# Kernel tuning notes

Hardware: AMD Instinct MI355X
Metric: run time of the kernel (lower is better)

The kernel has to match this reference:

```python
import jax, jax.numpy as jnp
import numpy as np

# Module hyper-parameters (init_kwargs)
CLIPVAR = 5.0   # variance is clipped to this before confidence = exp(-var)
MAXRANGE = 16   # max integration radius (pixels) in each of 4 directions
LAM = 0.05      # blend factor between depthin and CRF lateral estimate
N_CLASSES = 19


def _shift(x, axis, d, fill):
    """d=+1: out[..., n] = x[..., n-1] (pad with fill); d=-1: out[..., n] = x[..., n+1]."""
    pad = [(0, 0)] * x.ndim
    idx = [slice(None)] * x.ndim
    L = x.shape[axis]
    if d > 0:
        pad[axis] = (1, 0)
        idx[axis] = slice(0, L)
    else:
        pad[axis] = (0, 1)
        idx[axis] = slice(1, L + 1)
    return jnp.pad(x, pad, constant_values=fill)[tuple(idx)]


def _dir_accum(g, sem, msk, var, dep, axis, d, pre_shift, sign, clipvar, R):
    """Accumulate confidence-weighted depth estimates propagated from up to R
    same-semantic neighbors along one direction. All arrays are [bz,h,w].
    Depth estimate from neighbor at offset s: dep[neighbor] * exp(signed path
    sum of log-gradients g along the traversal)."""
    zeros = jnp.zeros_like(dep)
    valid0 = (msk == 1)  # only masked centers receive contributions

    def step(carry, _):
        g_sh, sem_sh, msk_sh, var_sh, dep_sh, pathlog, valid, dsum, csum = carry
        if pre_shift:  # newly added gradient term lives at the neighbor pixel
            g_sh = _shift(g_sh, axis, d, 0.0)
            pathlog = pathlog + sign * g_sh
        else:          # newly added gradient term lives one step before neighbor
            pathlog = pathlog + sign * g_sh
            g_sh = _shift(g_sh, axis, d, 0.0)
        sem_sh = _shift(sem_sh, axis, d, -1)
        msk_sh = _shift(msk_sh, axis, d, 0)
        var_sh = _shift(var_sh, axis, d, 0.0)
        dep_sh = _shift(dep_sh, axis, d, 0.0)
        # traversal stops (stays stopped) at semantic boundary / invalid pixel
        valid = valid & (sem_sh == sem) & (msk_sh == 1)
        conf = jnp.where(valid, jnp.exp(-jnp.minimum(var_sh, clipvar)), 0.0)
        dsum = dsum + conf * dep_sh * jnp.exp(pathlog)
        csum = csum + conf
        return (g_sh, sem_sh, msk_sh, var_sh, dep_sh, pathlog, valid, dsum, csum), None

    carry0 = (g, sem, msk, var, dep, zeros, valid0, zeros, zeros)
    carry, _ = jax.lax.scan(step, carry0, None, length=R)
    return carry[-2], carry[-1]


def crf_integrate(pred_log, semantics, mask, variance, depthin, clipvar, R):
    g0 = pred_log[:, 0]  # horizontal log-gradient: log d[n+1] - log d[n]
    g1 = pred_log[:, 1]  # vertical   log-gradient: log d[m+1] - log d[m]
    sem = semantics[:, 0]
    msk = mask[:, 0]
    var = variance[:, 0]
    dep = depthin[:, 0]
    # self term
    selfconf = jnp.where(msk == 1, jnp.exp(-jnp.minimum(var, clipvar)), 0.0)
    dsum = selfconf * dep
    csum = selfconf
    # (gradient map, axis, shift dir, pre_shift_g, sign): left, right, up, down
    dirs = [(g0, 2, 1, True, 1.0), (g0, 2, -1, False, -1.0),
            (g1, 1, 1, True, 1.0), (g1, 1, -1, False, -1.0)]
    for g, axis, d, pre, sgn in dirs:
        ds, cs = _dir_accum(g, sem, msk, var, dep, axis, d, pre, sgn, clipvar, R)
        dsum = dsum + ds
        csum = csum + cs
    out = jnp.where(csum > 0, dsum / jnp.maximum(csum, 1e-12), 0.0)
    return out[:, None]  # [bz,1,h,w]


def setup_inputs() -> dict:
    key = jax.random.key(0)
    k1, k2, k3, k4, k5 = jax.random.split(key, 5)
    bz, h, w = 4, 256, 832
    pred_log = 0.1 * jax.random.normal(k1, (bz, 2, h, w), dtype=jnp.float32)
    semantics = jax.random.randint(k2, (bz, 1, h, w), 0, N_CLASSES, dtype=jnp.int32)
    mask = jax.random.randint(k3, (bz, 1, h, w), 0, 2, dtype=jnp.int32)
    variance = 5.0 * jax.random.uniform(k4, (bz, 1, h, w), dtype=jnp.float32)
    depthin = 0.5 + 10.0 * jax.random.uniform(k5, (bz, 1, h, w), dtype=jnp.float32)
    return {"pred_log": pred_log, "semantics": semantics, "mask": mask,
            "variance": variance, "depthin": depthin, "times": 1}


def reference(pred_log, semantics, mask, variance, depthin, times):
    depthout = depthin
    for _ in range(times):
        lateral = crf_integrate(pred_log, semantics, mask, variance, depthout,
                                 CLIPVAR, MAXRANGE)
        sel = (lateral > 0).astype(depthin.dtype)
        depthout = (1.0 - sel) * depthin + sel * (depthin * LAM + lateral * (1.0 - LAM))
    return depthout
```

## Files before the change

### kernel.cpp

```cpp
#include <hip/hip_runtime.h>

#define W 832
#define H 256
#define BZ 4
#define RR 16
#define LAM_C 0.05f

#define CT 32
#define S  64
#define NT 512
#define NBLK (26 * 8 * 4)


__device__ __forceinline__ unsigned bf16r(float x) {
    const unsigned u = __float_as_uint(x);
    return (u + 0x7FFFu + ((u >> 16) & 1u)) >> 16;
}
__device__ __forceinline__ float decCD(unsigned p) {
    return __uint_as_float(p & 0xFFFF0000u);
}
__device__ __forceinline__ float decCF(unsigned p) {
    return __uint_as_float(0x3B800000u + ((p & 0xFFE0u) << 11));
}

__global__ __launch_bounds__(NT) void k_fused(
    const float* __restrict__ pred_log, const int* __restrict__ sem,
    const int* __restrict__ msk, const float* __restrict__ var,
    const float* __restrict__ dep, float* __restrict__ out)
{
    __shared__ float    sG0[S * S];
    __shared__ unsigned sP1[S * S];
    __shared__ float    sG1[S * CT];

    const int orig = blockIdx.x;
    const int wg   = (orig & 7) * 104 + (orig >> 3);
    const int bz   = wg / 208;
    const int rem  = wg - bz * 208;
    const int by   = rem / 26;
    const int bx   = rem - by * 26;

    const int tid = threadIdx.x;
    const int c0 = bx * CT;
    const int r0 = by * CT;
    const size_t im0 = (size_t)bz * H * W;
    const size_t g0b = ((size_t)(bz * 2)) * H * W;
    const size_t g1b = ((size_t)(bz * 2 + 1)) * H * W;

    #pragma unroll
    for (int k = 0; k < 2; ++k) {
        const int q = tid + NT * k;
        const int sr = q >> 4;
        const int sc4 = (q & 15) << 2;
        const int rimg = r0 - RR + sr;
        const int cimg = c0 - RR + sc4;
        float4 g4 = make_float4(0.f, 0.f, 0.f, 0.f);
        uint4 p4 = make_uint4(31u, 31u, 31u, 31u);
        if (rimg >= 0 && rimg < H && cimg >= 0 && cimg < W) {
            const size_t off = im0 + (size_t)rimg * W + cimg;
            g4 = *reinterpret_cast<const float4*>(&pred_log[g0b + (size_t)rimg * W + cimg]);
            const int4   mk4 = *reinterpret_cast<const int4*>(&msk[off]);
            const int4   se4 = *reinterpret_cast<const int4*>(&sem[off]);
            const float4 vr4 = *reinterpret_cast<const float4*>(&var[off]);
            const float4 dp4 = *reinterpret_cast<const float4*>(&dep[off]);
            #pragma unroll
            for (int e = 0; e < 4; ++e) {
                const int   mk1 = (&mk4.x)[e];
                const float vr1 = (&vr4.x)[e];
                if (mk1 == 1) {
                    const float cf = __expf(-fminf(vr1, 5.f));
                    const unsigned enc = (__float_as_uint(cf) - 0x3B800000u + 0x8000u) >> 16;
                    (&p4.x)[e] = (bf16r(cf * (&dp4.x)[e]) << 16) | (enc << 5)
                               | (unsigned)(&se4.x)[e];
                }
            }
        }
        const int i = sr * S + sc4;
        *reinterpret_cast<float4*>(&sG0[i]) = g4;
        *reinterpret_cast<uint4*>(&sP1[i])  = p4;
    }
    {
        const int ar = tid >> 3;
        const int ac4 = (tid & 7) << 2;
        const int rimg = r0 - RR + ar;
        float4 g1q = make_float4(0.f, 0.f, 0.f, 0.f);
        if (rimg >= 0 && rimg < H)
            g1q = *reinterpret_cast<const float4*>(
                &pred_log[g1b + (size_t)rimg * W + c0 + ac4]);
        *reinterpret_cast<float4*>(&sG1[ar * CT + ac4]) = g1q;
    }
    __syncthreads();

    float dsA[4], csA[4];
    #pragma unroll
    for (int k = 0; k < 4; ++k) {
        const int row = (tid >> 5) + 16 * k;
        const int col = tid & 31;
        const int ci = row * S + RR + col;
        const unsigned uc = sP1[ci];
        const unsigned semc = uc & 31u;
        float ds = 0.0f, cs = 0.0f;
        if (semc != 31u) {
            ds = decCD(uc);
            cs = decCF(uc);
            float psum = 0.0f;
            #pragma unroll 1
            for (int s = 1; s <= RR; ++s) {
                const unsigned u = sP1[ci - s];
                if ((u & 31u) != semc) break;
                psum += sG0[ci - s];
                ds = fmaf(decCD(u), __expf(psum), ds);
                cs += decCF(u);
            }
            psum = 0.0f;
            #pragma unroll 1
            for (int s = 1; s <= RR; ++s) {
                const unsigned u = sP1[ci + s];
                if ((u & 31u) != semc) break;
                psum -= sG0[ci + s - 1];
                ds = fmaf(decCD(u), __expf(psum), ds);
                cs += decCF(u);
            }
        }
        dsA[k] = ds; csA[k] = cs;
    }

    #pragma unroll
    for (int j = 0; j < 2; ++j) {
        const int prow = (tid >> 5) + 16 * j;
        const int pcol = tid & 31;
        const int rs = prow + RR;
        const int ci = rs * S + RR + pcol;
        const int gi = rs * CT + pcol;
        const unsigned uc = sP1[ci];
        const unsigned semc = uc & 31u;
        const size_t off = im0 + (size_t)(r0 + prow) * W + (c0 + pcol);
        const float dpin = dep[off];
        float ds = dsA[j + 1], cs = csA[j + 1];
        if (semc != 31u) {
            float psum = 0.0f;
            #pragma unroll 1
            for (int s = 1; s <= RR; ++s) {
                const unsigned u = sP1[ci - s * S];
                if ((u & 31u) != semc) break;
                psum += sG1[gi - s * CT];
                ds = fmaf(decCD(u), __expf(psum), ds);
                cs += decCF(u);
            }
            psum = 0.0f;
            #pragma unroll 1
            for (int s = 1; s <= RR; ++s) {
                const unsigned u = sP1[ci + s * S];
                if ((u & 31u) != semc) break;
                psum -= sG1[gi + (s - 1) * CT];
                ds = fmaf(decCD(u), __expf(psum), ds);
                cs += decCF(u);
            }
        }
        const float lat = (cs > 0.0f) ? (ds / fmaxf(cs, 1e-12f)) : 0.0f;
        out[off] = (lat > 0.0f) ? fmaf(lat, 1.0f - LAM_C, dpin * LAM_C) : dpin;
    }
}

extern "C" void kernel_launch(void* const* d_in, const int* in_sizes, int n_in,
                              void* d_out, int out_size, void* d_ws, size_t ws_size,
                              hipStream_t stream)
{
    const float* pred_log = (const float*)d_in[0];
    const int*   sem      = (const int*)d_in[1];
    const int*   msk      = (const int*)d_in[2];
    const float* var      = (const float*)d_in[3];
    const float* dep      = (const float*)d_in[4];

    float* out = (float*)d_out;

    hipLaunchKernelGGL(k_fused, dim3(NBLK), dim3(NT), 0, stream,
                       pred_log, sem, msk, var, dep, out);
}
```

Baseline: 14.91 us.

## Prepack per-pixel data in a separate kernel and trim redundant horizontal work

```diff
diff --git a/kernel.cpp b/kernel.cpp
--- a/kernel.cpp
+++ b/kernel.cpp
@@ -16,20 +16,47 @@
     const unsigned u = __float_as_uint(x);
     return (u + 0x7FFFu + ((u >> 16) & 1u)) >> 16;
 }
-__device__ __forceinline__ float decCD(unsigned p) {
+__device__ __forceinline__ float decDep(unsigned p) {
     return __uint_as_float(p & 0xFFFF0000u);
 }
 __device__ __forceinline__ float decCF(unsigned p) {
     return __uint_as_float(0x3B800000u + ((p & 0xFFE0u) << 11));
 }
 
+__global__ __launch_bounds__(256) void k_pack(
+    const int* __restrict__ sem, const int* __restrict__ msk,
+    const float* __restrict__ var, const float* __restrict__ dep,
+    uint4* __restrict__ p1)
+{
+    const int i = blockIdx.x * 256 + threadIdx.x;
+    const int4   mk4 = reinterpret_cast<const int4*>(msk)[i];
+    const int4   se4 = reinterpret_cast<const int4*>(sem)[i];
+    const float4 vr4 = reinterpret_cast<const float4*>(var)[i];
+    const float4 dp4 = reinterpret_cast<const float4*>(dep)[i];
+    uint4 p4;
+    #pragma unroll
+    for (int e = 0; e < 4; ++e) {
+        const float dpb = (float)(&dp4.x)[e];
+        unsigned w = bf16r(dpb) << 16;
+        if ((&mk4.x)[e] == 1) {
+            const float cf = __expf(-fminf((&vr4.x)[e], 5.f));
+            const unsigned enc = (__float_as_uint(cf) - 0x3B800000u + 0x8000u) >> 16;
+            w |= (enc << 5) | (unsigned)(&se4.x)[e];
+        } else {
+            w |= 31u;
+        }
+        (&p4.x)[e] = w;
+    }
+    p1[i] = p4;
+}
+
 __global__ __launch_bounds__(NT) void k_fused(
-    const float* __restrict__ pred_log, const int* __restrict__ sem,
-    const int* __restrict__ msk, const float* __restrict__ var,
-    const float* __restrict__ dep, float* __restrict__ out)
+    const float* __restrict__ pred_log,
+    const uint4* __restrict__ wsP1,
+    float* __restrict__ out)
 {
-    __shared__ float    sG0[S * S];
     __shared__ unsigned sP1[S * S];
+    __shared__ float    sG0[CT * S];
     __shared__ float    sG1[S * CT];
 
     const int orig = blockIdx.x;
@@ -42,9 +69,9 @@
     const int tid = threadIdx.x;
     const int c0 = bx * CT;
     const int r0 = by * CT;
-    const size_t im0 = (size_t)bz * H * W;
-    const size_t g0b = ((size_t)(bz * 2)) * H * W;
-    const size_t g1b = ((size_t)(bz * 2 + 1)) * H * W;
+    const int im0 = bz * (H * W);
+    const int g0b = (bz * 2) * (H * W);
+    const int g1b = (bz * 2 + 1) * (H * W);
 
     #pragma unroll
     for (int k = 0; k < 2; ++k) {
@@ -53,89 +80,81 @@
         const int sc4 = (q & 15) << 2;
         const int rimg = r0 - RR + sr;
         const int cimg = c0 - RR + sc4;
+        uint4 p4 = make_uint4(31u, 31u, 31u, 31u);
+        if ((unsigned)rimg < H && (unsigned)cimg < W)
+            p4 = wsP1[(im0 + rimg * W + cimg) >> 2];
+        *reinterpret_cast<uint4*>(&sP1[sr * S + sc4]) = p4;
+    }
+    {
+        const int sr = tid >> 4;
+        const int sc4 = (tid & 15) << 2;
+        const int cimg = c0 - RR + sc4;
         float4 g4 = make_float4(0.f, 0.f, 0.f, 0.f);
-        uint4 p4 = make_uint4(31u, 31u, 31u, 31u);
-        if (rimg >= 0 && rimg < H && cimg >= 0 && cimg < W) {
-            const size_t off = im0 + (size_t)rimg * W + cimg;
-            g4 = *reinterpret_cast<const float4*>(&pred_log[g0b + (size_t)rimg * W + cimg]);
-            const int4   mk4 = *reinterpret_cast<const int4*>(&msk[off]);
-            const int4   se4 = *reinterpret_cast<const int4*>(&sem[off]);
-            const float4 vr4 = *reinterpret_cast<const float4*>(&var[off]);
-            const float4 dp4 = *reinterpret_cast<const float4*>(&dep[off]);
-            #pragma unroll
-            for (int e = 0; e < 4; ++e) {
-                const int   mk1 = (&mk4.x)[e];
-                const float vr1 = (&vr4.x)[e];
-                if (mk1 == 1) {
-                    const float cf = __expf(-fminf(vr1, 5.f));
-                    const unsigned enc = (__float_as_uint(cf) - 0x3B800000u + 0x8000u) >> 16;
-                    (&p4.x)[e] = (bf16r(cf * (&dp4.x)[e]) << 16) | (enc << 5)
-                               | (unsigned)(&se4.x)[e];
-                }
-            }
-        }
-        const int i = sr * S + sc4;
-        *reinterpret_cast<float4*>(&sG0[i]) = g4;
-        *reinterpret_cast<uint4*>(&sP1[i])  = p4;
+        if ((unsigned)cimg < W)
+            g4 = *reinterpret_cast<const float4*>(
+                &pred_log[g0b + (r0 + sr) * W + cimg]);
+        *reinterpret_cast<float4*>(&sG0[sr * S + sc4]) = g4;
     }
     {
         const int ar = tid >> 3;
         const int ac4 = (tid & 7) << 2;
         const int rimg = r0 - RR + ar;
         float4 g1q = make_float4(0.f, 0.f, 0.f, 0.f);
-        if (rimg >= 0 && rimg < H)
+        if ((unsigned)rimg < H)
             g1q = *reinterpret_cast<const float4*>(
-                &pred_log[g1b + (size_t)rimg * W + c0 + ac4]);
+                &pred_log[g1b + rimg * W + c0 + ac4]);
         *reinterpret_cast<float4*>(&sG1[ar * CT + ac4]) = g1q;
     }
     __syncthreads();
 
-    float dsA[4], csA[4];
-    #pragma unroll
-    for (int k = 0; k < 4; ++k) {
-        const int row = (tid >> 5) + 16 * k;
-        const int col = tid & 31;
-        const int ci = row * S + RR + col;
+    const int cr0 = tid >> 5;
+    const int col = tid & 31;
+
+    float dsA[2], csA[2];
+    #pragma unroll
+    for (int j = 0; j < 2; ++j) {
+        const int cr = cr0 + 16 * j;
+        const int ci = (cr + RR) * S + RR + col;
+        const int gi = cr * S + RR + col;
         const unsigned uc = sP1[ci];
         const unsigned semc = uc & 31u;
         float ds = 0.0f, cs = 0.0f;
         if (semc != 31u) {
-            ds = decCD(uc);
-            cs = decCF(uc);
+            const float cfc = decCF(uc);
+            ds = cfc * decDep(uc);
+            cs = cfc;
             float psum = 0.0f;
             #pragma unroll 1
             for (int s = 1; s <= RR; ++s) {
                 const unsigned u = sP1[ci - s];
                 if ((u & 31u) != semc) break;
-                psum += sG0[ci - s];
-                ds = fmaf(decCD(u), __expf(psum), ds);
-                cs += decCF(u);
+                psum += sG0[gi - s];
+                const float cfn = decCF(u);
+                ds = fmaf(cfn * decDep(u), __expf(psum), ds);
+                cs += cfn;
             }
             psum = 0.0f;
             #pragma unroll 1
             for (int s = 1; s <= RR; ++s) {
                 const unsigned u = sP1[ci + s];
                 if ((u & 31u) != semc) break;
-                psum -= sG0[ci + s - 1];
-                ds = fmaf(decCD(u), __expf(psum), ds);
-                cs += decCF(u);
+                psum -= sG0[gi + s - 1];
+                const float cfn = decCF(u);
+                ds = fmaf(cfn * decDep(u), __expf(psum), ds);
+                cs += cfn;
             }
         }
-        dsA[k] = ds; csA[k] = cs;
+        dsA[j] = ds; csA[j] = cs;
     }
 
     #pragma unroll
     for (int j = 0; j < 2; ++j) {
-        const int prow = (tid >> 5) + 16 * j;
-        const int pcol = tid & 31;
-        const int rs = prow + RR;
-        const int ci = rs * S + RR + pcol;
-        const int gi = rs * CT + pcol;
+        const int cr = cr0 + 16 * j;
+        const int ci = (cr + RR) * S + RR + col;
+        const int gi = (cr + RR) * CT + col;
         const unsigned uc = sP1[ci];
         const unsigned semc = uc & 31u;
-        const size_t off = im0 + (size_t)(r0 + prow) * W + (c0 + pcol);
-        const float dpin = dep[off];
-        float ds = dsA[j + 1], cs = csA[j + 1];
+        float ds = dsA[j], cs = csA[j];
         if (semc != 31u) {
             float psum = 0.0f;
             #pragma unroll 1
@@ -143,8 +162,9 @@
                 const unsigned u = sP1[ci - s * S];
                 if ((u & 31u) != semc) break;
                 psum += sG1[gi - s * CT];
-                ds = fmaf(decCD(u), __expf(psum), ds);
-                cs += decCF(u);
+                const float cfn = decCF(u);
+                ds = fmaf(cfn * decDep(u), __expf(psum), ds);
+                cs += cfn;
             }
             psum = 0.0f;
             #pragma unroll 1
@@ -152,12 +172,15 @@
                 const unsigned u = sP1[ci + s * S];
                 if ((u & 31u) != semc) break;
                 psum -= sG1[gi + (s - 1) * CT];
-                ds = fmaf(decCD(u), __expf(psum), ds);
-                cs += decCF(u);
+                const float cfn = decCF(u);
+                ds = fmaf(cfn * decDep(u), __expf(psum), ds);
+                cs += cfn;
             }
         }
+        const float dpin = decDep(uc);
         const float lat = (cs > 0.0f) ? (ds / fmaxf(cs, 1e-12f)) : 0.0f;
-        out[off] = (lat > 0.0f) ? fmaf(lat, 1.0f - LAM_C, dpin * LAM_C) : dpin;
+        out[im0 + (r0 + cr) * W + c0 + col] =
+            (lat > 0.0f) ? fmaf(lat, 1.0f - LAM_C, dpin * LAM_C) : dpin;
     }
 }
 
@@ -172,7 +195,10 @@
     const float* dep      = (const float*)d_in[4];
 
     float* out = (float*)d_out;
-
+    uint4* wsP1 = (uint4*)d_ws;
+
+    hipLaunchKernelGGL(k_pack, dim3(BZ * H * W / 1024), dim3(256), 0, stream,
+                       sem, msk, var, dep, wsP1);
     hipLaunchKernelGGL(k_fused, dim3(NBLK), dim3(NT), 0, stream,
-                       pred_log, sem, msk, var, dep, out);
-}
+                       pred_log, wsP1, out);
+}
```

After: 17.19 us. +15.3%, slower.

## Drop gradient smem tiles, peel first two steps, skip halo-row horizontal passes

Applied to the files above, without the earlier changes.

```diff
diff --git a/kernel.cpp b/kernel.cpp
--- a/kernel.cpp
+++ b/kernel.cpp
@@ -16,7 +16,7 @@
     const unsigned u = __float_as_uint(x);
     return (u + 0x7FFFu + ((u >> 16) & 1u)) >> 16;
 }
-__device__ __forceinline__ float decCD(unsigned p) {
+__device__ __forceinline__ float decDep(unsigned p) {
     return __uint_as_float(p & 0xFFFF0000u);
 }
 __device__ __forceinline__ float decCF(unsigned p) {
@@ -28,9 +28,7 @@
     const int* __restrict__ msk, const float* __restrict__ var,
     const float* __restrict__ dep, float* __restrict__ out)
 {
-    __shared__ float    sG0[S * S];
     __shared__ unsigned sP1[S * S];
-    __shared__ float    sG1[S * CT];
 
     const int orig = blockIdx.x;
     const int wg   = (orig & 7) * 104 + (orig >> 3);
@@ -42,9 +40,9 @@
     const int tid = threadIdx.x;
     const int c0 = bx * CT;
     const int r0 = by * CT;
-    const size_t im0 = (size_t)bz * H * W;
-    const size_t g0b = ((size_t)(bz * 2)) * H * W;
-    const size_t g1b = ((size_t)(bz * 2 + 1)) * H * W;
+    const int im0 = bz * (H * W);
+    const float* g0p = pred_log + (size_t)(bz * 2) * (H * W);
+    const float* g1p = pred_log + (size_t)(bz * 2 + 1) * (H * W);
 
     #pragma unroll
     for (int k = 0; k < 2; ++k) {
@@ -53,111 +51,139 @@
         const int sc4 = (q & 15) << 2;
         const int rimg = r0 - RR + sr;
         const int cimg = c0 - RR + sc4;
-        float4 g4 = make_float4(0.f, 0.f, 0.f, 0.f);
         uint4 p4 = make_uint4(31u, 31u, 31u, 31u);
-        if (rimg >= 0 && rimg < H && cimg >= 0 && cimg < W) {
-            const size_t off = im0 + (size_t)rimg * W + cimg;
-            g4 = *reinterpret_cast<const float4*>(&pred_log[g0b + (size_t)rimg * W + cimg]);
+        if ((unsigned)rimg < H && (unsigned)cimg < W) {
+            const int off = im0 + rimg * W + cimg;
             const int4   mk4 = *reinterpret_cast<const int4*>(&msk[off]);
             const int4   se4 = *reinterpret_cast<const int4*>(&sem[off]);
             const float4 vr4 = *reinterpret_cast<const float4*>(&var[off]);
             const float4 dp4 = *reinterpret_cast<const float4*>(&dep[off]);
             #pragma unroll
             for (int e = 0; e < 4; ++e) {
-                const int   mk1 = (&mk4.x)[e];
-                const float vr1 = (&vr4.x)[e];
-                if (mk1 == 1) {
-                    const float cf = __expf(-fminf(vr1, 5.f));
-                    const unsigned enc = (__float_as_uint(cf) - 0x3B800000u + 0x8000u) >> 16;
-                    (&p4.x)[e] = (bf16r(cf * (&dp4.x)[e]) << 16) | (enc << 5)
-                               | (unsigned)(&se4.x)[e];
-                }
-            }
-        }
-        const int i = sr * S + sc4;
-        *reinterpret_cast<float4*>(&sG0[i]) = g4;
-        *reinterpret_cast<uint4*>(&sP1[i])  = p4;
-    }
-    {
-        const int ar = tid >> 3;
-        const int ac4 = (tid & 7) << 2;
-        const int rimg = r0 - RR + ar;
-        float4 g1q = make_float4(0.f, 0.f, 0.f, 0.f);
-        if (rimg >= 0 && rimg < H)
-            g1q = *reinterpret_cast<const float4*>(
-                &pred_log[g1b + (size_t)rimg * W + c0 + ac4]);
-        *reinterpret_cast<float4*>(&sG1[ar * CT + ac4]) = g1q;
+                unsigned w = bf16r((&dp4.x)[e]) << 16;
+                if ((&mk4.x)[e] == 1) {
+                    const float cf = __expf(-fminf((&vr4.x)[e], 5.f));
+                    const unsigned enc =
+                        (__float_as_uint(cf) - 0x3B800000u + 0x8000u) >> 16;
+                    w |= (enc << 5) | (unsigned)(&se4.x)[e];
+                } else w |= 31u;
+                (&p4.x)[e] = w;
+            }
+        }
+        *reinterpret_cast<uint4*>(&sP1[sr * S + sc4]) = p4;
     }
     __syncthreads();
 
-    float dsA[4], csA[4];
+    const int cr0 = tid >> 5;
+    const int col = tid & 31;
+
     #pragma unroll
-    for (int k = 0; k < 4; ++k) {
-        const int row = (tid >> 5) + 16 * k;
-        const int col = tid & 31;
-        const int ci = row * S + RR + col;
+    for (int j = 0; j < 2; ++j) {
+        const int cr = cr0 + 16 * j;
+        const int r  = r0 + cr;
+        const int c  = c0 + col;
+        const int rW = r * W;
+        const int ci = (cr + RR) * S + RR + col;
+
         const unsigned uc = sP1[ci];
         const unsigned semc = uc & 31u;
-        float ds = 0.0f, cs = 0.0f;
-        if (semc != 31u) {
-            ds = decCD(uc);
-            cs = decCF(uc);
-            float psum = 0.0f;
-            #pragma unroll 1
-            for (int s = 1; s <= RR; ++s) {
+        const bool alive = (semc != 31u);
+
+        const unsigned uL1 = sP1[ci - 1],     uL2 = sP1[ci - 2];
+        const unsigned uR1 = sP1[ci + 1],     uR2 = sP1[ci + 2];
+        const unsigned uU1 = sP1[ci - S],     uU2 = sP1[ci - 2 * S];
+        const unsigned uD1 = sP1[ci + S],     uD2 = sP1[ci + 2 * S];
+        const float gL1 = g0p[rW + max(c - 1, 0)];
+        const float gL2 = g0p[rW + max(c - 2, 0)];
+        const float gR1 = g0p[rW + c];
+        const float gR2 = g0p[rW + min(c + 1, W - 1)];
+        const float gU1 = g1p[max(r - 1, 0) * W + c];
+        const float gU2 = g1p[max(r - 2, 0) * W + c];
+        const float gD1 = g1p[rW + c];
+        const float gD2 = g1p[min(r + 1, H - 1) * W + c];
+
+        const bool vL1 = alive && ((uL1 & 31u) == semc);
+        const bool vR1 = alive && ((uR1 & 31u) == semc);
+        const bool vU1 = alive && ((uU1 & 31u) == semc);
+        const bool vD1 = alive && ((uD1 & 31u) == semc);
+        const bool vL2 = vL1 && ((uL2 & 31u) == semc);
+        const bool vR2 = vR1 && ((uR2 & 31u) == semc);
+        const bool vU2 = vU1 && ((uU2 & 31u) == semc);
+        const bool vD2 = vD1 && ((uD2 & 31u) == semc);
+
+        const float cfc = decCF(uc);
+        float ds = alive ? cfc * decDep(uc) : 0.0f;
+        float cs = alive ? cfc : 0.0f;
+
+        const float pL2 = gL1 + gL2, pR2 = -gR1 - gR2;
+        const float pU2 = gU1 + gU2, pD2 = -gD1 - gD2;
+
+        ds = fmaf(vL1 ? decCF(uL1) * decDep(uL1) : 0.f, __expf(gL1),  ds);
+        cs += vL1 ? decCF(uL1) : 0.f;
+        ds = fmaf(vL2 ? decCF(uL2) * decDep(uL2) : 0.f, __expf(pL2),  ds);
+        cs += vL2 ? decCF(uL2) : 0.f;
+        ds = fmaf(vR1 ? decCF(uR1) * decDep(uR1) : 0.f, __expf(-gR1), ds);
+        cs += vR1 ? decCF(uR1) : 0.f;
+        ds = fmaf(vR2 ? decCF(uR2) * decDep(uR2) : 0.f, __expf(pR2),  ds);
+        cs += vR2 ? decCF(uR2) : 0.f;
+        ds = fmaf(vU1 ? decCF(uU1) * decDep(uU1) : 0.f, __expf(gU1),  ds);
+        cs += vU1 ? decCF(uU1) : 0.f;
+        ds = fmaf(vU2 ? decCF(uU2) * decDep(uU2) : 0.f, __expf(pU2),  ds);
+        cs += vU2 ? decCF(uU2) : 0.f;
+        ds = fmaf(vD1 ? decCF(uD1) * decDep(uD1) : 0.f, __expf(-gD1), ds);
+        cs += vD1 ? decCF(uD1) : 0.f;
+        ds = fmaf(vD2 ? decCF(uD2) * decDep(uD2) : 0.f, __expf(pD2),  ds);
+        cs += vD2 ? decCF(uD2) : 0.f;
+
+        if (vL2) {
+            float psum = pL2;
+            #pragma unroll 1
+            for (int s = 3; s <= RR; ++s) {
                 const unsigned u = sP1[ci - s];
                 if ((u & 31u) != semc) break;
-                psum += sG0[ci - s];
-                ds = fmaf(decCD(u), __expf(psum), ds);
-                cs += decCF(u);
-            }
-            psum = 0.0f;
-            #pragma unroll 1
-            for (int s = 1; s <= RR; ++s) {
+                psum += g0p[rW + (c - s)];
+                ds = fmaf(decCF(u) * decDep(u), __expf(psum), ds);
+                cs += decCF(u);
+            }
+        }
+        if (vR2) {
+            float psum = pR2;
+            #pragma unroll 1
+            for (int s = 3; s <= RR; ++s) {
                 const unsigned u = sP1[ci + s];
                 if ((u & 31u) != semc) break;
-                psum -= sG0[ci + s - 1];
-                ds = fmaf(decCD(u), __expf(psum), ds);
-                cs += decCF(u);
-            }
-        }
-        dsA[k] = ds; csA[k] = cs;
-    }
-
-    #pragma unroll
-    for (int j = 0; j < 2; ++j) {
-        const int prow = (tid >> 5) + 16 * j;
-        const int pcol = tid & 31;
-        const int rs = prow + RR;
-        const int ci = rs * S + RR + pcol;
-        const int gi = rs * CT + pcol;
-        const unsigned uc = sP1[ci];
-        const unsigned semc = uc & 31u;
-        const size_t off = im0 + (size_t)(r0 + prow) * W + (c0 + pcol);
-        const float dpin = dep[off];
-        float ds = dsA[j + 1], cs = csA[j + 1];
-        if (semc != 31u) {
-            float psum = 0.0f;
-            #pragma unroll 1
-            for (int s = 1; s <= RR; ++s) {
+                psum -= g0p[rW + (c + s - 1)];
+                ds = fmaf(decCF(u) * decDep(u), __expf(psum), ds);
+                cs += decCF(u);
+            }
+        }
+        if (vU2) {
+            float psum = pU2;
+            #pragma unroll 1
+            for (int s = 3; s <= RR; ++s) {
                 const unsigned u = sP1[ci - s * S];
                 if ((u & 31u) != semc) break;
-                psum += sG1[gi - s * CT];
-                ds = fmaf(decCD(u), __expf(psum), ds);
-                cs += decCF(u);
-            }
-            psum = 0.0f;
-            #pragma unroll 1
-            for (int s = 1; s <= RR; ++s) {
+                psum += g1p[(r - s) * W + c];
+                ds = fmaf(decCF(u) * decDep(u), __expf(psum), ds);
+                cs += decCF(u);
+            }
+        }
+        if (vD2) {
+            float psum = pD2;
+            #pragma unroll 1
+            for (int s = 3; s <= RR; ++s) {
                 const unsigned u = sP1[ci + s * S];
                 if ((u & 31u) != semc) break;
-                psum -= sG1[gi + (s - 1) * CT];
-                ds = fmaf(decCD(u), __expf(psum), ds);
-                cs += decCF(u);
-            }
-        }
+                psum -= g1p[(r + s - 1) * W + c];
+                ds = fmaf(decCF(u) * decDep(u), __expf(psum), ds);
+                cs += decCF(u);
+            }
+        }
+
+        const float dpin = decDep(uc);
         const float lat = (cs > 0.0f) ? (ds / fmaxf(cs, 1e-12f)) : 0.0f;
-        out[off] = (lat > 0.0f) ? fmaf(lat, 1.0f - LAM_C, dpin * LAM_C) : dpin;
+        out[im0 + rW + c] =
+            (lat > 0.0f) ? fmaf(lat, 1.0f - LAM_C, dpin * LAM_C) : dpin;
     }
 }
 
```

After: 14.13 us. 1.05x faster.
